# Kernel optimization log

Hardware: AMD Instinct MI355X
Metric: run time of the kernel (lower is better)

## Reference

```python
import jax, jax.numpy as jnp
import numpy as np

N = 100000   # nodes
E = 3200000  # directed edges
F_IN = 128   # data.num_node_features
H = 16       # hidden
C = 2        # output classes (hard-coded in module)


def _glorot(key, fan_in, fan_out):
    s = jnp.sqrt(6.0 / (fan_in + fan_out)).astype(jnp.float32)
    return jax.random.uniform(key, (fan_in, fan_out), jnp.float32, -s, s)


def setup_inputs() -> dict:
    key = jax.random.key(0)
    ks = jax.random.split(key, 5)
    x = jax.random.normal(ks[0], (N, F_IN), jnp.float32)
    edge_index = jax.random.randint(ks[1], (2, E), 0, N, dtype=jnp.int64)
    return {
        "x": x,
        "edge_index": edge_index,
        "W1": _glorot(ks[2], F_IN, H), "b1": jnp.zeros((H,), jnp.float32),
        "W2": _glorot(ks[3], H, H),    "b2": jnp.zeros((H,), jnp.float32),
        "W3": _glorot(ks[4], H, C),    "b3": jnp.zeros((C,), jnp.float32),
    }


def _gcn_conv(x, W, b, src, dst, norm, n):
    # PyG GCNConv: linear transform, then normalized gather -> scatter-add, + bias
    h = x @ W                                   # [N, out]
    msg = h[src] * norm[:, None]                # [E+N, out] gather over source nodes
    out = jax.ops.segment_sum(msg, dst, num_segments=n)  # scatter-add at targets
    return out + b


def reference(x, edge_index, W1, b1, W2, b2, W3, b3):
    n = x.shape[0]
    loop = jnp.arange(n, dtype=edge_index.dtype)
    src = jnp.concatenate([edge_index[0], loop])  # add self-loops (PyG default)
    dst = jnp.concatenate([edge_index[1], loop])
    # symmetric normalization: deg^{-1/2}[src] * deg^{-1/2}[dst], deg = in-degree w/ self-loops
    deg = jax.ops.segment_sum(jnp.ones(src.shape, jnp.float32), dst, num_segments=n)
    dis = jnp.where(deg > 0, jax.lax.rsqrt(jnp.maximum(deg, 1.0)), 0.0)
    norm = dis[src] * dis[dst]
    # dropout is identity in eval mode
    h = jax.nn.relu(_gcn_conv(x, W1, b1, src, dst, norm, n))
    h = jax.nn.relu(_gcn_conv(h, W2, b2, src, dst, norm, n))
    h = _gcn_conv(h, W3, b3, src, dst, norm, n)
    return jax.nn.log_softmax(h, axis=1)
```

## Files before the change

### kernel.cpp

```cpp
#include <hip/hip_runtime.h>
#include <math.h>

#define NSB   512
#define BSH   8
#define BKN   256
#define ESMAX 6272
#define SLOT  10240

typedef _Float16 h8  __attribute__((ext_vector_type(8)));
typedef _Float16 h4  __attribute__((ext_vector_type(4)));
typedef _Float16 h2v __attribute__((ext_vector_type(2)));

__device__ inline int wave_scan_incl(int v) {
    int lane = threadIdx.x & 63;
#pragma unroll
    for (int d = 1; d < 64; d <<= 1) {
        int t = __shfl_up(v, d, 64);
        if (lane >= d) v += t;
    }
    return v;
}


__global__ void k_bucket(const int* __restrict__ src, const int* __restrict__ dst,
                         int* __restrict__ gcur, unsigned* __restrict__ col,
                         int e, int nbuck, int es) {
    __shared__ unsigned sorted[ESMAX];
    __shared__ unsigned char sbuck[ESMAX];
    __shared__ int lc[512], lofE[512], lcur[512], soff[512];
    __shared__ int wsum[8];
    int tid = threadIdx.x;
    lc[tid] = 0;
    __syncthreads();
    int lo = blockIdx.x * es;
    int hi = min(lo + es, e);
    for (int i = lo + tid; i < hi; i += 512)
        atomicAdd(&lc[dst[i] >> BSH], 1);
    __syncthreads();
    int c = lc[tid];
    int inc = wave_scan_incl(c);
    int wid = tid >> 6;
    if ((tid & 63) == 63) wsum[wid] = inc;
    __syncthreads();
    int wofs = 0;
#pragma unroll
    for (int w = 0; w < 8; w++) wofs += (w < wid) ? wsum[w] : 0;
    int excl = inc - c + wofs;
    lofE[tid] = excl;
    lcur[tid] = excl;
    if (tid < nbuck && c > 0)
        soff[tid] = tid * SLOT + atomicAdd(&gcur[tid], c);
    __syncthreads();
    for (int i = lo + tid; i < hi; i += 512) {
        int d = dst[i];
        int b = d >> BSH;
        int p = atomicAdd(&lcur[b], 1);
        sorted[p] = ((unsigned)src[i] << BSH) | (unsigned)(d & (BKN - 1));
        sbuck[p] = (unsigned char)(b & 255);
    }
    __syncthreads();
    int cnt_ = hi - lo;
    int split = (nbuck > 256) ? lofE[256] : 0x7fffffff;
    for (int i = tid; i < cnt_; i += 512) {
        int b = sbuck[i] | ((i >= split) ? 256 : 0);
        col[soff[b] + (i - lofE[b])] = sorted[i];
    }
}


__global__ __launch_bounds__(512) void k_sort(
        const unsigned* __restrict__ col, const int* __restrict__ gcur,
        int* __restrict__ col2, int* __restrict__ rs,
        int* __restrict__ re, float* __restrict__ dis,
        int n, int nbuck) {
    __shared__ int cnt[BKN];
    __shared__ int cur[BKN];
    __shared__ int wsum[4];
    __shared__ int sdat[SLOT];
    int tid = threadIdx.x;
    int b = blockIdx.x;
    int lo = b * SLOT;
    int tot = gcur[b];
    int hi = lo + tot;
    if (tid < BKN) cnt[tid] = 0;
    __syncthreads();
    for (int i = lo + tid; i < hi; i += 512)
        atomicAdd(&cnt[col[i] & (BKN - 1u)], 1);
    __syncthreads();
    int c = (tid < BKN) ? cnt[tid] : 0;
    int inc = wave_scan_incl(c);
    int wid = tid >> 6;
    if (tid < BKN && (tid & 63) == 63) wsum[wid] = inc;
    __syncthreads();
    if (tid < BKN) {
        int wofs = 0;
#pragma unroll
        for (int w = 0; w < 4; w++) wofs += (w < wid) ? wsum[w] : 0;
        int excl = inc - c + wofs;
        cur[tid] = excl;
        int node = (b << BSH) + tid;
        if (node < n) {
            rs[node] = lo + excl;
            re[node] = lo + excl + c;
            dis[node] = rsqrtf((float)(c + 1));
        }
    }
    __syncthreads();
    for (int i = lo + tid; i < hi; i += 512) {
        unsigned v = col[i];
        int pos = atomicAdd(&cur[v & (BKN - 1u)], 1);
        sdat[pos] = (int)(v >> BSH);
    }
    __syncthreads();
    for (int i = tid; i < tot; i += 512)
        col2[lo + i] = sdat[i];
}


__global__ __launch_bounds__(512) void k_linear1s(
        const float* __restrict__ x, const float* __restrict__ W,
        const float* __restrict__ dis, _Float16* __restrict__ hs, int n) {
    __shared__ float sW[2048];
    int tid = threadIdx.x;
    for (int i = tid; i < 2048; i += 512) sW[i] = W[i];
    __syncthreads();
    int cg = tid & 3;
    int kg = (tid >> 2) & 7;
    int nl = tid >> 5;
    float wr[16][4];
#pragma unroll
    for (int j = 0; j < 16; j++)
#pragma unroll
        for (int cc = 0; cc < 4; cc++)
            wr[j][cc] = sW[(kg * 16 + j) * 16 + cg * 4 + cc];
    int nodeBase = blockIdx.x * 128 + nl;
    for (int it = 0; it < 8; it++) {
        int node = nodeBase + it * 16;
        float a0 = 0.f, a1 = 0.f, a2 = 0.f, a3 = 0.f;
        if (node < n) {
            const float4* xr = (const float4*)(x + (size_t)node * 128 + kg * 16);
#pragma unroll
            for (int j4 = 0; j4 < 4; j4++) {
                float4 xv = xr[j4];
                float xs0 = xv.x, xs1 = xv.y, xs2 = xv.z, xs3 = xv.w;
                int j = j4 * 4;
                a0 += xs0 * wr[j][0] + xs1 * wr[j+1][0] + xs2 * wr[j+2][0] + xs3 * wr[j+3][0];
                a1 += xs0 * wr[j][1] + xs1 * wr[j+1][1] + xs2 * wr[j+2][1] + xs3 * wr[j+3][1];
                a2 += xs0 * wr[j][2] + xs1 * wr[j+1][2] + xs2 * wr[j+2][2] + xs3 * wr[j+3][2];
                a3 += xs0 * wr[j][3] + xs1 * wr[j+1][3] + xs2 * wr[j+2][3] + xs3 * wr[j+3][3];
            }
        }
#pragma unroll
        for (int m = 4; m <= 16; m <<= 1) {
            a0 += __shfl_xor(a0, m);
            a1 += __shfl_xor(a1, m);
            a2 += __shfl_xor(a2, m);
            a3 += __shfl_xor(a3, m);
        }
        if (kg == 0 && node < n) {
            float d = dis[node];
            h4 o;
            o[0] = (_Float16)(a0 * d);
            o[1] = (_Float16)(a1 * d);
            o[2] = (_Float16)(a2 * d);
            o[3] = (_Float16)(a3 * d);
            *((h4*)(hs + (size_t)node * 16 + cg * 4)) = o;
        }
    }
}


__global__ __launch_bounds__(256) void k_pullA(
        const _Float16* __restrict__ hs, const int* __restrict__ rs,
        const int* __restrict__ re, const int* __restrict__ col2,
        const float* __restrict__ dis, const float* __restrict__ bb,
        const float* __restrict__ W, _Float16* __restrict__ hsOut, int n) {
    __shared__ float sW[256];
    __shared__ float sb[16];
    if (threadIdx.x < 256) sW[threadIdx.x] = W[threadIdx.x];
    if (threadIdx.x < 16) sb[threadIdx.x] = bb[threadIdx.x];
    __syncthreads();
    long long t = (long long)blockIdx.x * blockDim.x + threadIdx.x;
    int node = (int)(t >> 2), qt = (int)(t & 3);
    if (node >= n) return;
    const h8* H = (const h8*)hs;
    float acc[16];
    if (qt == 0) {
        h8 s0 = H[(size_t)node * 2];
        h8 s1 = H[(size_t)node * 2 + 1];
#pragma unroll
        for (int j = 0; j < 8; j++) { acc[j] = (float)s0[j]; acc[8 + j] = (float)s1[j]; }
    } else {
#pragma unroll
        for (int j = 0; j < 16; j++) acc[j] = 0.f;
    }
    int b = rs[node], e2 = re[node];
    int i = b + qt;
    for (; i + 12 < e2; i += 16) {
        int s0 = col2[i], s1 = col2[i + 4], s2 = col2[i + 8], s3 = col2[i + 12];
        h8 a0 = H[(size_t)s0 * 2], b0 = H[(size_t)s0 * 2 + 1];
        h8 a1 = H[(size_t)s1 * 2], b1 = H[(size_t)s1 * 2 + 1];
        h8 a2 = H[(size_t)s2 * 2], b2 = H[(size_t)s2 * 2 + 1];
        h8 a3 = H[(size_t)s3 * 2], b3 = H[(size_t)s3 * 2 + 1];
#pragma unroll
        for (int j = 0; j < 8; j++) {
            acc[j]     += (float)a0[j] + (float)a1[j] + (float)a2[j] + (float)a3[j];
            acc[8 + j] += (float)b0[j] + (float)b1[j] + (float)b2[j] + (float)b3[j];
        }
    }
    for (; i < e2; i += 4) {
        int s = col2[i];
        h8 a = H[(size_t)s * 2], bq = H[(size_t)s * 2 + 1];
#pragma unroll
        for (int j = 0; j < 8; j++) { acc[j] += (float)a[j]; acc[8 + j] += (float)bq[j]; }
    }
#pragma unroll
    for (int j = 0; j < 16; j++) {
        acc[j] += __shfl_xor(acc[j], 1);
        acc[j] += __shfl_xor(acc[j], 2);
    }
    float d = dis[node];
    float va[16];
#pragma unroll
    for (int k = 0; k < 16; k++) {
        float v = acc[k] * d + sb[k];
        va[k] = v > 0.f ? v : 0.f;
    }
    h4 o;
#pragma unroll
    for (int cc = 0; cc < 4; cc++) {
        int cidx = (qt << 2) + cc;
        float s = 0.f;
#pragma unroll
        for (int k = 0; k < 16; k++) s += va[k] * sW[k * 16 + cidx];
        o[cc] = (_Float16)(s * d);
    }
    *((h4*)(hsOut + (size_t)node * 16 + (qt << 2))) = o;
}


__global__ __launch_bounds__(256) void k_pullB(
        const _Float16* __restrict__ hs, const int* __restrict__ rs,
        const int* __restrict__ re, const int* __restrict__ col2,
        const float* __restrict__ dis, const float* __restrict__ bb,
        const float* __restrict__ W, _Float16* __restrict__ hs2, int n) {
    __shared__ float sW[32];
    __shared__ float sb[16];
    if (threadIdx.x < 32) sW[threadIdx.x] = W[threadIdx.x];
    if (threadIdx.x < 16) sb[threadIdx.x] = bb[threadIdx.x];
    __syncthreads();
    long long t = (long long)blockIdx.x * blockDim.x + threadIdx.x;
    int node = (int)(t >> 2), qt = (int)(t & 3);
    if (node >= n) return;
    const h8* H = (const h8*)hs;
    float acc[16];
    if (qt == 0) {
        h8 s0 = H[(size_t)node * 2];
        h8 s1 = H[(size_t)node * 2 + 1];
#pragma unroll
        for (int j = 0; j < 8; j++) { acc[j] = (float)s0[j]; acc[8 + j] = (float)s1[j]; }
    } else {
#pragma unroll
        for (int j = 0; j < 16; j++) acc[j] = 0.f;
    }
    int b = rs[node], e2 = re[node];
    int i = b + qt;
    for (; i + 12 < e2; i += 16) {
        int s0 = col2[i], s1 = col2[i + 4], s2 = col2[i + 8], s3 = col2[i + 12];
        h8 a0 = H[(size_t)s0 * 2], b0 = H[(size_t)s0 * 2 + 1];
        h8 a1 = H[(size_t)s1 * 2], b1 = H[(size_t)s1 * 2 + 1];
        h8 a2 = H[(size_t)s2 * 2], b2 = H[(size_t)s2 * 2 + 1];
        h8 a3 = H[(size_t)s3 * 2], b3 = H[(size_t)s3 * 2 + 1];
#pragma unroll
        for (int j = 0; j < 8; j++) {
            acc[j]     += (float)a0[j] + (float)a1[j] + (float)a2[j] + (float)a3[j];
            acc[8 + j] += (float)b0[j] + (float)b1[j] + (float)b2[j] + (float)b3[j];
        }
    }
    for (; i < e2; i += 4) {
        int s = col2[i];
        h8 a = H[(size_t)s * 2], bq = H[(size_t)s * 2 + 1];
#pragma unroll
        for (int j = 0; j < 8; j++) { acc[j] += (float)a[j]; acc[8 + j] += (float)bq[j]; }
    }
#pragma unroll
    for (int j = 0; j < 16; j++) {
        acc[j] += __shfl_xor(acc[j], 1);
        acc[j] += __shfl_xor(acc[j], 2);
    }
    float d = dis[node];
    float p0 = 0.f, p1 = 0.f;
#pragma unroll
    for (int k = 0; k < 16; k++) {
        float v = acc[k] * d + sb[k];
        v = v > 0.f ? v : 0.f;
        p0 += v * sW[k * 2 + 0];
        p1 += v * sW[k * 2 + 1];
    }
    if (qt == 0) {
        h2v o;
        o[0] = (_Float16)(p0 * d);
        o[1] = (_Float16)(p1 * d);
        ((h2v*)hs2)[node] = o;
    }
}


__global__ __launch_bounds__(256) void k_pull2lsm(
        const _Float16* __restrict__ hs2, const int* __restrict__ rs,
        const int* __restrict__ re, const int* __restrict__ col2,
        const float* __restrict__ dis, const float* __restrict__ b3,
        float* __restrict__ out, int n) {
    long long t = (long long)blockIdx.x * blockDim.x + threadIdx.x;
    int node = (int)(t >> 2), qt = (int)(t & 3);
    if (node >= n) return;
    const h2v* H = (const h2v*)hs2;
    float a0 = 0.f, a1 = 0.f;
    if (qt == 0) {
        h2v self = H[node];
        a0 = (float)self[0]; a1 = (float)self[1];
    }
    int b = rs[node], e2 = re[node];
    int i = b + qt;
    for (; i + 12 < e2; i += 16) {
        h2v v0 = H[col2[i]];
        h2v v1 = H[col2[i + 4]];
        h2v v2 = H[col2[i + 8]];
        h2v v3 = H[col2[i + 12]];
        a0 += (float)v0[0] + (float)v1[0] + (float)v2[0] + (float)v3[0];
        a1 += (float)v0[1] + (float)v1[1] + (float)v2[1] + (float)v3[1];
    }
    for (; i < e2; i += 4) {
        h2v v = H[col2[i]];
        a0 += (float)v[0];
        a1 += (float)v[1];
    }
    a0 += __shfl_xor(a0, 1); a0 += __shfl_xor(a0, 2);
    a1 += __shfl_xor(a1, 1); a1 += __shfl_xor(a1, 2);
    if (qt == 0) {
        float d = dis[node];
        float z0 = a0 * d + b3[0];
        float z1 = a1 * d + b3[1];
        float m = fmaxf(z0, z1);
        float l = m + logf(expf(z0 - m) + expf(z1 - m));
        float2 o = {z0 - l, z1 - l};
        ((float2*)out)[node] = o;
    }
}


extern "C" void kernel_launch(void* const* d_in, const int* in_sizes, int n_in,
                              void* d_out, int out_size, void* d_ws, size_t ws_size,
                              hipStream_t stream) {
    const float* x  = (const float*)d_in[0];
    const int*   ei = (const int*)d_in[1];
    const float* W1 = (const float*)d_in[2];
    const float* b1 = (const float*)d_in[3];
    const float* W2 = (const float*)d_in[4];
    const float* b2 = (const float*)d_in[5];
    const float* W3 = (const float*)d_in[6];
    const float* b3 = (const float*)d_in[7];
    float* out = (float*)d_out;

    const int N = in_sizes[0] / 128;
    const int E = in_sizes[1] / 2;
    const int* src = ei;
    const int* dst = ei + E;

    const int NBUCK = (N + BKN - 1) >> BSH;
    const int ES = (E + NSB - 1) / NSB;

    char* ws = (char*)d_ws;
    size_t off = 0;
    auto alloc = [&](size_t bytes) {
        void* p = ws + off;
        off += (bytes + 255) & ~(size_t)255;
        return p;
    };
    int*       gcur = (int*)alloc((size_t)NBUCK * sizeof(int));
    unsigned*  col  = (unsigned*)alloc((size_t)NBUCK * SLOT * sizeof(unsigned));
    int*       col2 = (int*)alloc((size_t)NBUCK * SLOT * sizeof(int));
    int*       rs   = (int*)alloc((size_t)N * sizeof(int));
    int*       re   = (int*)alloc((size_t)N * sizeof(int));
    float*     dis  = (float*)alloc((size_t)N * sizeof(float));
    _Float16*  hsA  = (_Float16*)alloc((size_t)N * 16 * sizeof(_Float16));
    _Float16*  hsB  = (_Float16*)alloc((size_t)N * 16 * sizeof(_Float16));
    _Float16*  hs2  = (_Float16*)alloc((size_t)N * 2 * sizeof(_Float16));

    const int B = 256;
    auto g = [&](long long work) { return (int)((work + B - 1) / B); };

    hipMemsetAsync(gcur, 0, (size_t)NBUCK * sizeof(int), stream);
    k_bucket<<<NSB, 512, 0, stream>>>(src, dst, gcur, col, E, NBUCK, ES);
    k_sort<<<NBUCK, 512, 0, stream>>>(col, gcur, col2, rs, re, dis, N, NBUCK);

    k_linear1s<<<(N + 127) / 128, 512, 0, stream>>>(x, W1, dis, hsA, N);

    k_pullA<<<g((long long)N * 4), B, 0, stream>>>(hsA, rs, re, col2, dis, b1, W2, hsB, N);

    k_pullB<<<g((long long)N * 4), B, 0, stream>>>(hsB, rs, re, col2, dis, b2, W3, hs2, N);

    k_pull2lsm<<<g((long long)N * 4), B, 0, stream>>>(hs2, rs, re, col2, dis, b3, out, N);
}
```

Measured before the change: 247.8 us.

## Fuse all pipeline stages into one persistent cooperative kernel with grid syncs

Replaces the memset plus six separate kernel launches with a single cooperative persistent kernel. Grid-stride loops cover each stage, grid-wide barriers separate the stages, and a shared-memory union serves every stage. The aim is to remove per-launch overhead and the idle gaps between the small kernels. In exchange, occupancy is capped by the largest stage's shared-memory footprint and launch bounds, and each grid sync costs time.

```diff
diff --git a/kernel.cpp b/kernel.cpp
--- a/kernel.cpp
+++ b/kernel.cpp
@@ -1,4 +1,5 @@
 #include <hip/hip_runtime.h>
+#include <hip/hip_cooperative_groups.h>
 #include <math.h>
 
 #define NSB   512
@@ -11,6 +12,22 @@
 typedef _Float16 h4  __attribute__((ext_vector_type(4)));
 typedef _Float16 h2v __attribute__((ext_vector_type(2)));
 
+union SU {
+    struct {
+        unsigned sorted[ESMAX];
+        int lc[512], lofE[512], lcur[512], soff[512];
+        int wsum[8];
+        unsigned char sbuck[ESMAX];
+    } b;
+    struct {
+        int sdat[SLOT];
+        int cnt[BKN], cur[BKN];
+        int wsum[4];
+    } s;
+    struct { float sW[2048]; } l;
+    struct { float sW[256]; float sb[16]; } p;
+};
+
 __device__ inline int wave_scan_incl(int v) {
     int lane = threadIdx.x & 63;
 #pragma unroll
@@ -21,330 +38,326 @@
     return v;
 }
 
-
-__global__ void k_bucket(const int* __restrict__ src, const int* __restrict__ dst,
-                         int* __restrict__ gcur, unsigned* __restrict__ col,
-                         int e, int nbuck, int es) {
-    __shared__ unsigned sorted[ESMAX];
-    __shared__ unsigned char sbuck[ESMAX];
-    __shared__ int lc[512], lofE[512], lcur[512], soff[512];
-    __shared__ int wsum[8];
+__device__ inline void gsync(cooperative_groups::grid_group& g) {
+    __threadfence();
+    g.sync();
+    __threadfence();
+}
+
+
+__global__ __launch_bounds__(512, 4) void k_mega(
+        const float* __restrict__ x, const int* __restrict__ srcv, const int* __restrict__ dstv,
+        const float* __restrict__ W1, const float* __restrict__ bias1,
+        const float* __restrict__ W2, const float* __restrict__ bias2,
+        const float* __restrict__ W3, const float* __restrict__ bias3,
+        int* __restrict__ gcur, unsigned* __restrict__ col, int* __restrict__ col2,
+        int* __restrict__ rs, int* __restrict__ re, float* __restrict__ dis,
+        _Float16* __restrict__ hsA, _Float16* __restrict__ hsB, _Float16* __restrict__ hs2,
+        float* __restrict__ out, int n, int e, int nbuck, int es)
+{
+    cooperative_groups::grid_group grid = cooperative_groups::this_grid();
+    __shared__ SU su;
     int tid = threadIdx.x;
-    lc[tid] = 0;
-    __syncthreads();
-    int lo = blockIdx.x * es;
-    int hi = min(lo + es, e);
-    for (int i = lo + tid; i < hi; i += 512)
-        atomicAdd(&lc[dst[i] >> BSH], 1);
-    __syncthreads();
-    int c = lc[tid];
-    int inc = wave_scan_incl(c);
-    int wid = tid >> 6;
-    if ((tid & 63) == 63) wsum[wid] = inc;
-    __syncthreads();
-    int wofs = 0;
-#pragma unroll
-    for (int w = 0; w < 8; w++) wofs += (w < wid) ? wsum[w] : 0;
-    int excl = inc - c + wofs;
-    lofE[tid] = excl;
-    lcur[tid] = excl;
-    if (tid < nbuck && c > 0)
-        soff[tid] = tid * SLOT + atomicAdd(&gcur[tid], c);
-    __syncthreads();
-    for (int i = lo + tid; i < hi; i += 512) {
-        int d = dst[i];
-        int b = d >> BSH;
-        int p = atomicAdd(&lcur[b], 1);
-        sorted[p] = ((unsigned)src[i] << BSH) | (unsigned)(d & (BKN - 1));
-        sbuck[p] = (unsigned char)(b & 255);
-    }
-    __syncthreads();
-    int cnt_ = hi - lo;
-    int split = (nbuck > 256) ? lofE[256] : 0x7fffffff;
-    for (int i = tid; i < cnt_; i += 512) {
-        int b = sbuck[i] | ((i >= split) ? 256 : 0);
-        col[soff[b] + (i - lofE[b])] = sorted[i];
-    }
-}
-
-
-__global__ __launch_bounds__(512) void k_sort(
-        const unsigned* __restrict__ col, const int* __restrict__ gcur,
-        int* __restrict__ col2, int* __restrict__ rs,
-        int* __restrict__ re, float* __restrict__ dis,
-        int n, int nbuck) {
-    __shared__ int cnt[BKN];
-    __shared__ int cur[BKN];
-    __shared__ int wsum[4];
-    __shared__ int sdat[SLOT];
-    int tid = threadIdx.x;
-    int b = blockIdx.x;
-    int lo = b * SLOT;
-    int tot = gcur[b];
-    int hi = lo + tot;
-    if (tid < BKN) cnt[tid] = 0;
-    __syncthreads();
-    for (int i = lo + tid; i < hi; i += 512)
-        atomicAdd(&cnt[col[i] & (BKN - 1u)], 1);
-    __syncthreads();
-    int c = (tid < BKN) ? cnt[tid] : 0;
-    int inc = wave_scan_incl(c);
-    int wid = tid >> 6;
-    if (tid < BKN && (tid & 63) == 63) wsum[wid] = inc;
-    __syncthreads();
-    if (tid < BKN) {
+
+    for (int i = blockIdx.x * 512 + tid; i < nbuck; i += gridDim.x * 512)
+        gcur[i] = 0;
+    gsync(grid);
+
+    for (int blk = blockIdx.x; blk * es < e; blk += gridDim.x) {
+        su.b.lc[tid] = 0;
+        __syncthreads();
+        int lo = blk * es;
+        int hi = min(lo + es, e);
+        for (int i = lo + tid; i < hi; i += 512)
+            atomicAdd(&su.b.lc[dstv[i] >> BSH], 1);
+        __syncthreads();
+        int c = su.b.lc[tid];
+        int inc = wave_scan_incl(c);
+        int wid = tid >> 6;
+        if ((tid & 63) == 63) su.b.wsum[wid] = inc;
+        __syncthreads();
         int wofs = 0;
 #pragma unroll
-        for (int w = 0; w < 4; w++) wofs += (w < wid) ? wsum[w] : 0;
+        for (int w = 0; w < 8; w++) wofs += (w < wid) ? su.b.wsum[w] : 0;
         int excl = inc - c + wofs;
-        cur[tid] = excl;
-        int node = (b << BSH) + tid;
-        if (node < n) {
-            rs[node] = lo + excl;
-            re[node] = lo + excl + c;
-            dis[node] = rsqrtf((float)(c + 1));
-        }
-    }
-    __syncthreads();
-    for (int i = lo + tid; i < hi; i += 512) {
-        unsigned v = col[i];
-        int pos = atomicAdd(&cur[v & (BKN - 1u)], 1);
-        sdat[pos] = (int)(v >> BSH);
-    }
-    __syncthreads();
-    for (int i = tid; i < tot; i += 512)
-        col2[lo + i] = sdat[i];
-}
-
-
-__global__ __launch_bounds__(512) void k_linear1s(
-        const float* __restrict__ x, const float* __restrict__ W,
-        const float* __restrict__ dis, _Float16* __restrict__ hs, int n) {
-    __shared__ float sW[2048];
-    int tid = threadIdx.x;
-    for (int i = tid; i < 2048; i += 512) sW[i] = W[i];
-    __syncthreads();
-    int cg = tid & 3;
-    int kg = (tid >> 2) & 7;
-    int nl = tid >> 5;
-    float wr[16][4];
-#pragma unroll
-    for (int j = 0; j < 16; j++)
-#pragma unroll
-        for (int cc = 0; cc < 4; cc++)
-            wr[j][cc] = sW[(kg * 16 + j) * 16 + cg * 4 + cc];
-    int nodeBase = blockIdx.x * 128 + nl;
-    for (int it = 0; it < 8; it++) {
-        int node = nodeBase + it * 16;
-        float a0 = 0.f, a1 = 0.f, a2 = 0.f, a3 = 0.f;
-        if (node < n) {
-            const float4* xr = (const float4*)(x + (size_t)node * 128 + kg * 16);
-#pragma unroll
-            for (int j4 = 0; j4 < 4; j4++) {
-                float4 xv = xr[j4];
-                float xs0 = xv.x, xs1 = xv.y, xs2 = xv.z, xs3 = xv.w;
-                int j = j4 * 4;
-                a0 += xs0 * wr[j][0] + xs1 * wr[j+1][0] + xs2 * wr[j+2][0] + xs3 * wr[j+3][0];
-                a1 += xs0 * wr[j][1] + xs1 * wr[j+1][1] + xs2 * wr[j+2][1] + xs3 * wr[j+3][1];
-                a2 += xs0 * wr[j][2] + xs1 * wr[j+1][2] + xs2 * wr[j+2][2] + xs3 * wr[j+3][2];
-                a3 += xs0 * wr[j][3] + xs1 * wr[j+1][3] + xs2 * wr[j+2][3] + xs3 * wr[j+3][3];
-            }
-        }
-#pragma unroll
-        for (int m = 4; m <= 16; m <<= 1) {
-            a0 += __shfl_xor(a0, m);
-            a1 += __shfl_xor(a1, m);
-            a2 += __shfl_xor(a2, m);
-            a3 += __shfl_xor(a3, m);
-        }
-        if (kg == 0 && node < n) {
+        su.b.lofE[tid] = excl;
+        su.b.lcur[tid] = excl;
+        if (tid < nbuck && c > 0)
+            su.b.soff[tid] = tid * SLOT + atomicAdd(&gcur[tid], c);
+        __syncthreads();
+        for (int i = lo + tid; i < hi; i += 512) {
+            int d = dstv[i];
+            int bb = d >> BSH;
+            int p = atomicAdd(&su.b.lcur[bb], 1);
+            su.b.sorted[p] = ((unsigned)srcv[i] << BSH) | (unsigned)(d & (BKN - 1));
+            su.b.sbuck[p] = (unsigned char)(bb & 255);
+        }
+        __syncthreads();
+        int cnt_ = hi - lo;
+        int split = (nbuck > 256) ? su.b.lofE[256] : 0x7fffffff;
+        for (int i = tid; i < cnt_; i += 512) {
+            int bb = su.b.sbuck[i] | ((i >= split) ? 256 : 0);
+            col[su.b.soff[bb] + (i - su.b.lofE[bb])] = su.b.sorted[i];
+        }
+        __syncthreads();
+    }
+    gsync(grid);
+
+    for (int bk = blockIdx.x; bk < nbuck; bk += gridDim.x) {
+        int lo = bk * SLOT;
+        int tot = gcur[bk];
+        int hi = lo + tot;
+        if (tid < BKN) su.s.cnt[tid] = 0;
+        __syncthreads();
+        for (int i = lo + tid; i < hi; i += 512)
+            atomicAdd(&su.s.cnt[col[i] & (BKN - 1u)], 1);
+        __syncthreads();
+        int c = (tid < BKN) ? su.s.cnt[tid] : 0;
+        int inc = wave_scan_incl(c);
+        int wid = tid >> 6;
+        if (tid < BKN && (tid & 63) == 63) su.s.wsum[wid] = inc;
+        __syncthreads();
+        if (tid < BKN) {
+            int wofs = 0;
+#pragma unroll
+            for (int w = 0; w < 4; w++) wofs += (w < wid) ? su.s.wsum[w] : 0;
+            int excl = inc - c + wofs;
+            su.s.cur[tid] = excl;
+            int node = (bk << BSH) + tid;
+            if (node < n) {
+                rs[node] = lo + excl;
+                re[node] = lo + excl + c;
+                dis[node] = rsqrtf((float)(c + 1));
+            }
+        }
+        __syncthreads();
+        for (int i = lo + tid; i < hi; i += 512) {
+            unsigned v = col[i];
+            int pos = atomicAdd(&su.s.cur[v & (BKN - 1u)], 1);
+            su.s.sdat[pos] = (int)(v >> BSH);
+        }
+        __syncthreads();
+        for (int i = tid; i < tot; i += 512)
+            col2[lo + i] = su.s.sdat[i];
+        __syncthreads();
+    }
+    gsync(grid);
+
+    {
+        for (int i = tid; i < 2048; i += 512) su.l.sW[i] = W1[i];
+        __syncthreads();
+        int cgi = tid & 3;
+        int kg = (tid >> 2) & 7;
+        int nl = tid >> 5;
+        float wr[16][4];
+#pragma unroll
+        for (int j = 0; j < 16; j++)
+#pragma unroll
+            for (int cc = 0; cc < 4; cc++)
+                wr[j][cc] = su.l.sW[(kg * 16 + j) * 16 + cgi * 4 + cc];
+        for (int base = blockIdx.x * 128; base < n; base += gridDim.x * 128) {
+            int nodeBase = base + nl;
+            for (int it = 0; it < 8; it++) {
+                int node = nodeBase + it * 16;
+                float a0 = 0.f, a1 = 0.f, a2 = 0.f, a3 = 0.f;
+                if (node < n) {
+                    const float4* xr = (const float4*)(x + (size_t)node * 128 + kg * 16);
+#pragma unroll
+                    for (int j4 = 0; j4 < 4; j4++) {
+                        float4 xv = xr[j4];
+                        float xs0 = xv.x, xs1 = xv.y, xs2 = xv.z, xs3 = xv.w;
+                        int j = j4 * 4;
+                        a0 += xs0 * wr[j][0] + xs1 * wr[j+1][0] + xs2 * wr[j+2][0] + xs3 * wr[j+3][0];
+                        a1 += xs0 * wr[j][1] + xs1 * wr[j+1][1] + xs2 * wr[j+2][1] + xs3 * wr[j+3][1];
+                        a2 += xs0 * wr[j][2] + xs1 * wr[j+1][2] + xs2 * wr[j+2][2] + xs3 * wr[j+3][2];
+                        a3 += xs0 * wr[j][3] + xs1 * wr[j+1][3] + xs2 * wr[j+2][3] + xs3 * wr[j+3][3];
+                    }
+                }
+#pragma unroll
+                for (int m = 4; m <= 16; m <<= 1) {
+                    a0 += __shfl_xor(a0, m);
+                    a1 += __shfl_xor(a1, m);
+                    a2 += __shfl_xor(a2, m);
+                    a3 += __shfl_xor(a3, m);
+                }
+                if (kg == 0 && node < n) {
+                    float d = dis[node];
+                    h4 o;
+                    o[0] = (_Float16)(a0 * d);
+                    o[1] = (_Float16)(a1 * d);
+                    o[2] = (_Float16)(a2 * d);
+                    o[3] = (_Float16)(a3 * d);
+                    *((h4*)(hsA + (size_t)node * 16 + cgi * 4)) = o;
+                }
+            }
+        }
+    }
+    gsync(grid);
+
+    {
+        if (tid < 256) su.p.sW[tid] = W2[tid];
+        if (tid < 16)  su.p.sb[tid] = bias1[tid];
+        __syncthreads();
+        const h8* H = (const h8*)hsA;
+        long long stride = (long long)gridDim.x * 512;
+        for (long long t = (long long)blockIdx.x * 512 + tid; (t >> 2) < (long long)n; t += stride) {
+            int node = (int)(t >> 2), qt = (int)(t & 3);
+            float acc[16];
+            if (qt == 0) {
+                h8 s0 = H[(size_t)node * 2];
+                h8 s1 = H[(size_t)node * 2 + 1];
+#pragma unroll
+                for (int j = 0; j < 8; j++) { acc[j] = (float)s0[j]; acc[8 + j] = (float)s1[j]; }
+            } else {
+#pragma unroll
+                for (int j = 0; j < 16; j++) acc[j] = 0.f;
+            }
+            int b0i = rs[node], e2 = re[node];
+            int i = b0i + qt;
+            for (; i + 12 < e2; i += 16) {
+                int s0 = col2[i], s1 = col2[i + 4], s2 = col2[i + 8], s3 = col2[i + 12];
+                h8 y0 = H[(size_t)s0 * 2], z0 = H[(size_t)s0 * 2 + 1];
+                h8 y1 = H[(size_t)s1 * 2], z1 = H[(size_t)s1 * 2 + 1];
+                h8 y2 = H[(size_t)s2 * 2], z2 = H[(size_t)s2 * 2 + 1];
+                h8 y3 = H[(size_t)s3 * 2], z3 = H[(size_t)s3 * 2 + 1];
+#pragma unroll
+                for (int j = 0; j < 8; j++) {
+                    acc[j]     += (float)y0[j] + (float)y1[j] + (float)y2[j] + (float)y3[j];
+                    acc[8 + j] += (float)z0[j] + (float)z1[j] + (float)z2[j] + (float)z3[j];
+                }
+            }
+            for (; i < e2; i += 4) {
+                int s = col2[i];
+                h8 y = H[(size_t)s * 2], z = H[(size_t)s * 2 + 1];
+#pragma unroll
+                for (int j = 0; j < 8; j++) { acc[j] += (float)y[j]; acc[8 + j] += (float)z[j]; }
+            }
+#pragma unroll
+            for (int j = 0; j < 16; j++) {
+                acc[j] += __shfl_xor(acc[j], 1);
+                acc[j] += __shfl_xor(acc[j], 2);
+            }
             float d = dis[node];
+            float va[16];
+#pragma unroll
+            for (int k = 0; k < 16; k++) {
+                float v = acc[k] * d + su.p.sb[k];
+                va[k] = v > 0.f ? v : 0.f;
+            }
             h4 o;
-            o[0] = (_Float16)(a0 * d);
-            o[1] = (_Float16)(a1 * d);
-            o[2] = (_Float16)(a2 * d);
-            o[3] = (_Float16)(a3 * d);
-            *((h4*)(hs + (size_t)node * 16 + cg * 4)) = o;
-        }
-    }
-}
-
-
-__global__ __launch_bounds__(256) void k_pullA(
-        const _Float16* __restrict__ hs, const int* __restrict__ rs,
-        const int* __restrict__ re, const int* __restrict__ col2,
-        const float* __restrict__ dis, const float* __restrict__ bb,
-        const float* __restrict__ W, _Float16* __restrict__ hsOut, int n) {
-    __shared__ float sW[256];
-    __shared__ float sb[16];
-    if (threadIdx.x < 256) sW[threadIdx.x] = W[threadIdx.x];
-    if (threadIdx.x < 16) sb[threadIdx.x] = bb[threadIdx.x];
-    __syncthreads();
-    long long t = (long long)blockIdx.x * blockDim.x + threadIdx.x;
-    int node = (int)(t >> 2), qt = (int)(t & 3);
-    if (node >= n) return;
-    const h8* H = (const h8*)hs;
-    float acc[16];
-    if (qt == 0) {
-        h8 s0 = H[(size_t)node * 2];
-        h8 s1 = H[(size_t)node * 2 + 1];
-#pragma unroll
-        for (int j = 0; j < 8; j++) { acc[j] = (float)s0[j]; acc[8 + j] = (float)s1[j]; }
-    } else {
-#pragma unroll
-        for (int j = 0; j < 16; j++) acc[j] = 0.f;
-    }
-    int b = rs[node], e2 = re[node];
-    int i = b + qt;
-    for (; i + 12 < e2; i += 16) {
-        int s0 = col2[i], s1 = col2[i + 4], s2 = col2[i + 8], s3 = col2[i + 12];
-        h8 a0 = H[(size_t)s0 * 2], b0 = H[(size_t)s0 * 2 + 1];
-        h8 a1 = H[(size_t)s1 * 2], b1 = H[(size_t)s1 * 2 + 1];
-        h8 a2 = H[(size_t)s2 * 2], b2 = H[(size_t)s2 * 2 + 1];
-        h8 a3 = H[(size_t)s3 * 2], b3 = H[(size_t)s3 * 2 + 1];
-#pragma unroll
-        for (int j = 0; j < 8; j++) {
-            acc[j]     += (float)a0[j] + (float)a1[j] + (float)a2[j] + (float)a3[j];
-            acc[8 + j] += (float)b0[j] + (float)b1[j] + (float)b2[j] + (float)b3[j];
-        }
-    }
-    for (; i < e2; i += 4) {
-        int s = col2[i];
-        h8 a = H[(size_t)s * 2], bq = H[(size_t)s * 2 + 1];
-#pragma unroll
-        for (int j = 0; j < 8; j++) { acc[j] += (float)a[j]; acc[8 + j] += (float)bq[j]; }
-    }
-#pragma unroll
-    for (int j = 0; j < 16; j++) {
-        acc[j] += __shfl_xor(acc[j], 1);
-        acc[j] += __shfl_xor(acc[j], 2);
-    }
-    float d = dis[node];
-    float va[16];
-#pragma unroll
-    for (int k = 0; k < 16; k++) {
-        float v = acc[k] * d + sb[k];
-        va[k] = v > 0.f ? v : 0.f;
-    }
-    h4 o;
-#pragma unroll
-    for (int cc = 0; cc < 4; cc++) {
-        int cidx = (qt << 2) + cc;
-        float s = 0.f;
-#pragma unroll
-        for (int k = 0; k < 16; k++) s += va[k] * sW[k * 16 + cidx];
-        o[cc] = (_Float16)(s * d);
-    }
-    *((h4*)(hsOut + (size_t)node * 16 + (qt << 2))) = o;
-}
-
-
-__global__ __launch_bounds__(256) void k_pullB(
-        const _Float16* __restrict__ hs, const int* __restrict__ rs,
-        const int* __restrict__ re, const int* __restrict__ col2,
-        const float* __restrict__ dis, const float* __restrict__ bb,
-        const float* __restrict__ W, _Float16* __restrict__ hs2, int n) {
-    __shared__ float sW[32];
-    __shared__ float sb[16];
-    if (threadIdx.x < 32) sW[threadIdx.x] = W[threadIdx.x];
-    if (threadIdx.x < 16) sb[threadIdx.x] = bb[threadIdx.x];
-    __syncthreads();
-    long long t = (long long)blockIdx.x * blockDim.x + threadIdx.x;
-    int node = (int)(t >> 2), qt = (int)(t & 3);
-    if (node >= n) return;
-    const h8* H = (const h8*)hs;
-    float acc[16];
-    if (qt == 0) {
-        h8 s0 = H[(size_t)node * 2];
-        h8 s1 = H[(size_t)node * 2 + 1];
-#pragma unroll
-        for (int j = 0; j < 8; j++) { acc[j] = (float)s0[j]; acc[8 + j] = (float)s1[j]; }
-    } else {
-#pragma unroll
-        for (int j = 0; j < 16; j++) acc[j] = 0.f;
-    }
-    int b = rs[node], e2 = re[node];
-    int i = b + qt;
-    for (; i + 12 < e2; i += 16) {
-        int s0 = col2[i], s1 = col2[i + 4], s2 = col2[i + 8], s3 = col2[i + 12];
-        h8 a0 = H[(size_t)s0 * 2], b0 = H[(size_t)s0 * 2 + 1];
-        h8 a1 = H[(size_t)s1 * 2], b1 = H[(size_t)s1 * 2 + 1];
-        h8 a2 = H[(size_t)s2 * 2], b2 = H[(size_t)s2 * 2 + 1];
-        h8 a3 = H[(size_t)s3 * 2], b3 = H[(size_t)s3 * 2 + 1];
-#pragma unroll
-        for (int j = 0; j < 8; j++) {
-            acc[j]     += (float)a0[j] + (float)a1[j] + (float)a2[j] + (float)a3[j];
-            acc[8 + j] += (float)b0[j] + (float)b1[j] + (float)b2[j] + (float)b3[j];
-        }
-    }
-    for (; i < e2; i += 4) {
-        int s = col2[i];
-        h8 a = H[(size_t)s * 2], bq = H[(size_t)s * 2 + 1];
-#pragma unroll
-        for (int j = 0; j < 8; j++) { acc[j] += (float)a[j]; acc[8 + j] += (float)bq[j]; }
-    }
-#pragma unroll
-    for (int j = 0; j < 16; j++) {
-        acc[j] += __shfl_xor(acc[j], 1);
-        acc[j] += __shfl_xor(acc[j], 2);
-    }
-    float d = dis[node];
-    float p0 = 0.f, p1 = 0.f;
-#pragma unroll
-    for (int k = 0; k < 16; k++) {
-        float v = acc[k] * d + sb[k];
-        v = v > 0.f ? v : 0.f;
-        p0 += v * sW[k * 2 + 0];
-        p1 += v * sW[k * 2 + 1];
-    }
-    if (qt == 0) {
-        h2v o;
-        o[0] = (_Float16)(p0 * d);
-        o[1] = (_Float16)(p1 * d);
-        ((h2v*)hs2)[node] = o;
-    }
-}
-
-
-__global__ __launch_bounds__(256) void k_pull2lsm(
-        const _Float16* __restrict__ hs2, const int* __restrict__ rs,
-        const int* __restrict__ re, const int* __restrict__ col2,
-        const float* __restrict__ dis, const float* __restrict__ b3,
-        float* __restrict__ out, int n) {
-    long long t = (long long)blockIdx.x * blockDim.x + threadIdx.x;
-    int node = (int)(t >> 2), qt = (int)(t & 3);
-    if (node >= n) return;
-    const h2v* H = (const h2v*)hs2;
-    float a0 = 0.f, a1 = 0.f;
-    if (qt == 0) {
-        h2v self = H[node];
-        a0 = (float)self[0]; a1 = (float)self[1];
-    }
-    int b = rs[node], e2 = re[node];
-    int i = b + qt;
-    for (; i + 12 < e2; i += 16) {
-        h2v v0 = H[col2[i]];
-        h2v v1 = H[col2[i + 4]];
-        h2v v2 = H[col2[i + 8]];
-        h2v v3 = H[col2[i + 12]];
-        a0 += (float)v0[0] + (float)v1[0] + (float)v2[0] + (float)v3[0];
-        a1 += (float)v0[1] + (float)v1[1] + (float)v2[1] + (float)v3[1];
-    }
-    for (; i < e2; i += 4) {
-        h2v v = H[col2[i]];
-        a0 += (float)v[0];
-        a1 += (float)v[1];
-    }
-    a0 += __shfl_xor(a0, 1); a0 += __shfl_xor(a0, 2);
-    a1 += __shfl_xor(a1, 1); a1 += __shfl_xor(a1, 2);
-    if (qt == 0) {
-        float d = dis[node];
-        float z0 = a0 * d + b3[0];
-        float z1 = a1 * d + b3[1];
-        float m = fmaxf(z0, z1);
-        float l = m + logf(expf(z0 - m) + expf(z1 - m));
-        float2 o = {z0 - l, z1 - l};
-        ((float2*)out)[node] = o;
+#pragma unroll
+            for (int cc = 0; cc < 4; cc++) {
+                int cidx = (qt << 2) + cc;
+                float s = 0.f;
+#pragma unroll
+                for (int k = 0; k < 16; k++) s += va[k] * su.p.sW[k * 16 + cidx];
+                o[cc] = (_Float16)(s * d);
+            }
+            *((h4*)(hsB + (size_t)node * 16 + (qt << 2))) = o;
+        }
+    }
+    gsync(grid);
+
+    {
+        if (tid < 32) su.p.sW[tid] = W3[tid];
+        if (tid < 16) su.p.sb[tid] = bias2[tid];
+        __syncthreads();
+        const h8* H = (const h8*)hsB;
+        long long stride = (long long)gridDim.x * 512;
+        for (long long t = (long long)blockIdx.x * 512 + tid; (t >> 2) < (long long)n; t += stride) {
+            int node = (int)(t >> 2), qt = (int)(t & 3);
+            float acc[16];
+            if (qt == 0) {
+                h8 s0 = H[(size_t)node * 2];
+                h8 s1 = H[(size_t)node * 2 + 1];
+#pragma unroll
+                for (int j = 0; j < 8; j++) { acc[j] = (float)s0[j]; acc[8 + j] = (float)s1[j]; }
+            } else {
+#pragma unroll
+                for (int j = 0; j < 16; j++) acc[j] = 0.f;
+            }
+            int b0i = rs[node], e2 = re[node];
+            int i = b0i + qt;
+            for (; i + 12 < e2; i += 16) {
+                int s0 = col2[i], s1 = col2[i + 4], s2 = col2[i + 8], s3 = col2[i + 12];
+                h8 y0 = H[(size_t)s0 * 2], z0 = H[(size_t)s0 * 2 + 1];
+                h8 y1 = H[(size_t)s1 * 2], z1 = H[(size_t)s1 * 2 + 1];
+                h8 y2 = H[(size_t)s2 * 2], z2 = H[(size_t)s2 * 2 + 1];
+                h8 y3 = H[(size_t)s3 * 2], z3 = H[(size_t)s3 * 2 + 1];
+#pragma unroll
+                for (int j = 0; j < 8; j++) {
+                    acc[j]     += (float)y0[j] + (float)y1[j] + (float)y2[j] + (float)y3[j];
+                    acc[8 + j] += (float)z0[j] + (float)z1[j] + (float)z2[j] + (float)z3[j];
+                }
+            }
+            for (; i < e2; i += 4) {
+                int s = col2[i];
+                h8 y = H[(size_t)s * 2], z = H[(size_t)s * 2 + 1];
+#pragma unroll
+                for (int j = 0; j < 8; j++) { acc[j] += (float)y[j]; acc[8 + j] += (float)z[j]; }
+            }
+#pragma unroll
+            for (int j = 0; j < 16; j++) {
+                acc[j] += __shfl_xor(acc[j], 1);
+                acc[j] += __shfl_xor(acc[j], 2);
+            }
+            float d = dis[node];
+            float p0 = 0.f, p1 = 0.f;
+#pragma unroll
+            for (int k = 0; k < 16; k++) {
+                float v = acc[k] * d + su.p.sb[k];
+                v = v > 0.f ? v : 0.f;
+                p0 += v * su.p.sW[k * 2 + 0];
+                p1 += v * su.p.sW[k * 2 + 1];
+            }
+            if (qt == 0) {
+                h2v o;
+                o[0] = (_Float16)(p0 * d);
+                o[1] = (_Float16)(p1 * d);
+                ((h2v*)hs2)[node] = o;
+            }
+        }
+    }
+    gsync(grid);
+
+    {
+        const h2v* H = (const h2v*)hs2;
+        float bz0 = bias3[0], bz1 = bias3[1];
+        long long stride = (long long)gridDim.x * 512;
+        for (long long t = (long long)blockIdx.x * 512 + tid; (t >> 2) < (long long)n; t += stride) {
+            int node = (int)(t >> 2), qt = (int)(t & 3);
+            float a0 = 0.f, a1 = 0.f;
+            if (qt == 0) {
+                h2v self = H[node];
+                a0 = (float)self[0]; a1 = (float)self[1];
+            }
+            int b0i = rs[node], e2 = re[node];
+            int i = b0i + qt;
+            for (; i + 12 < e2; i += 16) {
+                h2v v0 = H[col2[i]];
+                h2v v1 = H[col2[i + 4]];
+                h2v v2 = H[col2[i + 8]];
+                h2v v3 = H[col2[i + 12]];
+                a0 += (float)v0[0] + (float)v1[0] + (float)v2[0] + (float)v3[0];
+                a1 += (float)v0[1] + (float)v1[1] + (float)v2[1] + (float)v3[1];
+            }
+            for (; i < e2; i += 4) {
+                h2v v = H[col2[i]];
+                a0 += (float)v[0];
+                a1 += (float)v[1];
+            }
+            a0 += __shfl_xor(a0, 1); a0 += __shfl_xor(a0, 2);
+            a1 += __shfl_xor(a1, 1); a1 += __shfl_xor(a1, 2);
+            if (qt == 0) {
+                float d = dis[node];
+                float z0 = a0 * d + bz0;
+                float z1 = a1 * d + bz1;
+                float m = fmaxf(z0, z1);
+                float l = m + logf(expf(z0 - m) + expf(z1 - m));
+                float2 o = {z0 - l, z1 - l};
+                ((float2*)out)[node] = o;
+            }
+        }
     }
 }
 
@@ -362,13 +375,13 @@
     const float* b3 = (const float*)d_in[7];
     float* out = (float*)d_out;
 
-    const int N = in_sizes[0] / 128;
-    const int E = in_sizes[1] / 2;
+    int N = in_sizes[0] / 128;
+    int E = in_sizes[1] / 2;
     const int* src = ei;
     const int* dst = ei + E;
 
-    const int NBUCK = (N + BKN - 1) >> BSH;
-    const int ES = (E + NSB - 1) / NSB;
+    int NBUCK = (N + BKN - 1) >> BSH;
+    int ES = (E + NSB - 1) / NSB;
 
     char* ws = (char*)d_ws;
     size_t off = 0;
@@ -387,18 +400,23 @@
     _Float16*  hsB  = (_Float16*)alloc((size_t)N * 16 * sizeof(_Float16));
     _Float16*  hs2  = (_Float16*)alloc((size_t)N * 2 * sizeof(_Float16));
 
-    const int B = 256;
-    auto g = [&](long long work) { return (int)((work + B - 1) / B); };
-
-    hipMemsetAsync(gcur, 0, (size_t)NBUCK * sizeof(int), stream);
-    k_bucket<<<NSB, 512, 0, stream>>>(src, dst, gcur, col, E, NBUCK, ES);
-    k_sort<<<NBUCK, 512, 0, stream>>>(col, gcur, col2, rs, re, dis, N, NBUCK);
-
-    k_linear1s<<<(N + 127) / 128, 512, 0, stream>>>(x, W1, dis, hsA, N);
-
-    k_pullA<<<g((long long)N * 4), B, 0, stream>>>(hsA, rs, re, col2, dis, b1, W2, hsB, N);
-
-    k_pullB<<<g((long long)N * 4), B, 0, stream>>>(hsB, rs, re, col2, dis, b2, W3, hs2, N);
-
-    k_pull2lsm<<<g((long long)N * 4), B, 0, stream>>>(hs2, rs, re, col2, dis, b3, out, N);
+    static int gridBlocks = 0;
+    if (gridBlocks == 0) {
+        int mb = 0;
+        if (hipOccupancyMaxActiveBlocksPerMultiprocessor(&mb, k_mega, 512, 0) != hipSuccess || mb < 1)
+            mb = 2;
+        int ncu = 256;
+        int dev = 0;
+        hipGetDevice(&dev);
+        hipDeviceGetAttribute(&ncu, hipDeviceAttributeMultiprocessorCount, dev);
+        long long g = (long long)mb * ncu;
+        if (g > 1024) g = 1024;
+        gridBlocks = (int)g;
+    }
+
+    void* args[] = { &x, &src, &dst, &W1, &b1, &W2, &b2, &W3, &b3,
+                     &gcur, &col, &col2, &rs, &re, &dis, &hsA, &hsB, &hs2,
+                     &out, &N, &E, &NBUCK, &ES };
+    hipLaunchCooperativeKernel((void*)k_mega, dim3(gridBlocks), dim3(512),
+                               args, 0, stream);
 }
```

Result: slower. 898.3 us (+262.5%).

## Overlap first-layer linear with edge bucketing in one fused launch

Applied to the files above, without the earlier changes.

The edge-bucketing kernel and the first linear transform are merged into one launch with a block-index split. The extra blocks compute an unnormalized x@W1 while the bucket blocks run, so the two independent stages share the device instead of running back to back. Scaling by deg^-1/2 moves into the sort kernel, which also writes col2 straight to global memory instead of staging it in shared memory. The cost is an extra fp16 round trip through an hsRaw buffer and a larger shared-memory union that may reduce occupancy for the linear blocks.

```diff
diff --git a/kernel.cpp b/kernel.cpp
--- a/kernel.cpp
+++ b/kernel.cpp
@@ -22,66 +22,122 @@
 }
 
 
-__global__ void k_bucket(const int* __restrict__ src, const int* __restrict__ dst,
-                         int* __restrict__ gcur, unsigned* __restrict__ col,
-                         int e, int nbuck, int es) {
-    __shared__ unsigned sorted[ESMAX];
-    __shared__ unsigned char sbuck[ESMAX];
-    __shared__ int lc[512], lofE[512], lcur[512], soff[512];
-    __shared__ int wsum[8];
+union BU {
+    struct {
+        unsigned sorted[ESMAX];
+        int lc[512], lofE[512], lcur[512], soff[512];
+        int wsum[8];
+        unsigned char sbuck[ESMAX];
+    } b;
+    struct { float sW[2048]; } l;
+};
+
+__global__ __launch_bounds__(512) void k_build(
+        const int* __restrict__ srcv, const int* __restrict__ dstv,
+        const float* __restrict__ x, const float* __restrict__ W1,
+        int* __restrict__ gcur, unsigned* __restrict__ col,
+        _Float16* __restrict__ hsRaw,
+        int e, int nbuck, int es, int n, int nlin) {
+    __shared__ BU su;
     int tid = threadIdx.x;
-    lc[tid] = 0;
-    __syncthreads();
-    int lo = blockIdx.x * es;
-    int hi = min(lo + es, e);
-    for (int i = lo + tid; i < hi; i += 512)
-        atomicAdd(&lc[dst[i] >> BSH], 1);
-    __syncthreads();
-    int c = lc[tid];
-    int inc = wave_scan_incl(c);
-    int wid = tid >> 6;
-    if ((tid & 63) == 63) wsum[wid] = inc;
-    __syncthreads();
-    int wofs = 0;
-#pragma unroll
-    for (int w = 0; w < 8; w++) wofs += (w < wid) ? wsum[w] : 0;
-    int excl = inc - c + wofs;
-    lofE[tid] = excl;
-    lcur[tid] = excl;
-    if (tid < nbuck && c > 0)
-        soff[tid] = tid * SLOT + atomicAdd(&gcur[tid], c);
-    __syncthreads();
-    for (int i = lo + tid; i < hi; i += 512) {
-        int d = dst[i];
-        int b = d >> BSH;
-        int p = atomicAdd(&lcur[b], 1);
-        sorted[p] = ((unsigned)src[i] << BSH) | (unsigned)(d & (BKN - 1));
-        sbuck[p] = (unsigned char)(b & 255);
-    }
-    __syncthreads();
-    int cnt_ = hi - lo;
-    int split = (nbuck > 256) ? lofE[256] : 0x7fffffff;
-    for (int i = tid; i < cnt_; i += 512) {
-        int b = sbuck[i] | ((i >= split) ? 256 : 0);
-        col[soff[b] + (i - lofE[b])] = sorted[i];
-    }
-}
-
-
-__global__ __launch_bounds__(512) void k_sort(
+
+    if (blockIdx.x < NSB) {
+        su.b.lc[tid] = 0;
+        __syncthreads();
+        int lo = blockIdx.x * es;
+        int hi = min(lo + es, e);
+        for (int i = lo + tid; i < hi; i += 512)
+            atomicAdd(&su.b.lc[dstv[i] >> BSH], 1);
+        __syncthreads();
+        int c = su.b.lc[tid];
+        int inc = wave_scan_incl(c);
+        int wid = tid >> 6;
+        if ((tid & 63) == 63) su.b.wsum[wid] = inc;
+        __syncthreads();
+        int wofs = 0;
+#pragma unroll
+        for (int w = 0; w < 8; w++) wofs += (w < wid) ? su.b.wsum[w] : 0;
+        int excl = inc - c + wofs;
+        su.b.lofE[tid] = excl;
+        su.b.lcur[tid] = excl;
+        if (tid < nbuck && c > 0)
+            su.b.soff[tid] = tid * SLOT + atomicAdd(&gcur[tid], c);
+        __syncthreads();
+        for (int i = lo + tid; i < hi; i += 512) {
+            int d = dstv[i];
+            int bb = d >> BSH;
+            int p = atomicAdd(&su.b.lcur[bb], 1);
+            su.b.sorted[p] = ((unsigned)srcv[i] << BSH) | (unsigned)(d & (BKN - 1));
+            su.b.sbuck[p] = (unsigned char)(bb & 255);
+        }
+        __syncthreads();
+        int cnt_ = hi - lo;
+        int split = (nbuck > 256) ? su.b.lofE[256] : 0x7fffffff;
+        for (int i = tid; i < cnt_; i += 512) {
+            int bb = su.b.sbuck[i] | ((i >= split) ? 256 : 0);
+            col[su.b.soff[bb] + (i - su.b.lofE[bb])] = su.b.sorted[i];
+        }
+    } else {
+        for (int i = tid; i < 2048; i += 512) su.l.sW[i] = W1[i];
+        __syncthreads();
+        int cgi = tid & 3;
+        int kg  = (tid >> 2) & 15;
+        int wv  = tid >> 6;
+        float wr[8][4];
+#pragma unroll
+        for (int j = 0; j < 8; j++)
+#pragma unroll
+            for (int cc = 0; cc < 4; cc++)
+                wr[j][cc] = su.l.sW[(kg * 8 + j) * 16 + cgi * 4 + cc];
+        int lb = blockIdx.x - NSB;
+        for (int base = lb * 8; base < n; base += nlin * 8) {
+            int node = base + wv;
+            float a0 = 0.f, a1 = 0.f, a2 = 0.f, a3 = 0.f;
+            if (node < n) {
+                const float4* xr = (const float4*)(x + (size_t)node * 128 + kg * 8);
+                float4 xv0 = xr[0], xv1 = xr[1];
+                float xs[8] = {xv0.x, xv0.y, xv0.z, xv0.w, xv1.x, xv1.y, xv1.z, xv1.w};
+#pragma unroll
+                for (int j = 0; j < 8; j++) {
+                    a0 += xs[j] * wr[j][0];
+                    a1 += xs[j] * wr[j][1];
+                    a2 += xs[j] * wr[j][2];
+                    a3 += xs[j] * wr[j][3];
+                }
+            }
+#pragma unroll
+            for (int m = 4; m <= 32; m <<= 1) {
+                a0 += __shfl_xor(a0, m);
+                a1 += __shfl_xor(a1, m);
+                a2 += __shfl_xor(a2, m);
+                a3 += __shfl_xor(a3, m);
+            }
+            if (kg == 0 && node < n) {
+                h4 o;
+                o[0] = (_Float16)a0;
+                o[1] = (_Float16)a1;
+                o[2] = (_Float16)a2;
+                o[3] = (_Float16)a3;
+                *((h4*)(hsRaw + (size_t)node * 16 + cgi * 4)) = o;
+            }
+        }
+    }
+}
+
+
+__global__ __launch_bounds__(512) void k_sort2(
         const unsigned* __restrict__ col, const int* __restrict__ gcur,
         int* __restrict__ col2, int* __restrict__ rs,
         int* __restrict__ re, float* __restrict__ dis,
-        int n, int nbuck) {
+        const _Float16* __restrict__ hsRaw, _Float16* __restrict__ hsA, int n) {
     __shared__ int cnt[BKN];
     __shared__ int cur[BKN];
     __shared__ int wsum[4];
-    __shared__ int sdat[SLOT];
+    __shared__ float sdis[BKN];
     int tid = threadIdx.x;
-    int b = blockIdx.x;
-    int lo = b * SLOT;
-    int tot = gcur[b];
-    int hi = lo + tot;
+    int bk = blockIdx.x;
+    int lo = bk * SLOT;
+    int hi = lo + gcur[bk];
     if (tid < BKN) cnt[tid] = 0;
     __syncthreads();
     for (int i = lo + tid; i < hi; i += 512)
@@ -97,74 +153,31 @@
 #pragma unroll
         for (int w = 0; w < 4; w++) wofs += (w < wid) ? wsum[w] : 0;
         int excl = inc - c + wofs;
-        cur[tid] = excl;
-        int node = (b << BSH) + tid;
+        cur[tid] = lo + excl;
+        float d = rsqrtf((float)(c + 1));
+        sdis[tid] = d;
+        int node = (bk << BSH) + tid;
         if (node < n) {
             rs[node] = lo + excl;
             re[node] = lo + excl + c;
-            dis[node] = rsqrtf((float)(c + 1));
+            dis[node] = d;
         }
     }
     __syncthreads();
     for (int i = lo + tid; i < hi; i += 512) {
         unsigned v = col[i];
         int pos = atomicAdd(&cur[v & (BKN - 1u)], 1);
-        sdat[pos] = (int)(v >> BSH);
-    }
-    __syncthreads();
-    for (int i = tid; i < tot; i += 512)
-        col2[lo + i] = sdat[i];
-}
-
-
-__global__ __launch_bounds__(512) void k_linear1s(
-        const float* __restrict__ x, const float* __restrict__ W,
-        const float* __restrict__ dis, _Float16* __restrict__ hs, int n) {
-    __shared__ float sW[2048];
-    int tid = threadIdx.x;
-    for (int i = tid; i < 2048; i += 512) sW[i] = W[i];
-    __syncthreads();
-    int cg = tid & 3;
-    int kg = (tid >> 2) & 7;
-    int nl = tid >> 5;
-    float wr[16][4];
-#pragma unroll
-    for (int j = 0; j < 16; j++)
-#pragma unroll
-        for (int cc = 0; cc < 4; cc++)
-            wr[j][cc] = sW[(kg * 16 + j) * 16 + cg * 4 + cc];
-    int nodeBase = blockIdx.x * 128 + nl;
-    for (int it = 0; it < 8; it++) {
-        int node = nodeBase + it * 16;
-        float a0 = 0.f, a1 = 0.f, a2 = 0.f, a3 = 0.f;
+        col2[pos] = (int)(v >> BSH);
+    }
+    {
+        int node = (bk << BSH) + (tid >> 1);
         if (node < n) {
-            const float4* xr = (const float4*)(x + (size_t)node * 128 + kg * 16);
-#pragma unroll
-            for (int j4 = 0; j4 < 4; j4++) {
-                float4 xv = xr[j4];
-                float xs0 = xv.x, xs1 = xv.y, xs2 = xv.z, xs3 = xv.w;
-                int j = j4 * 4;
-                a0 += xs0 * wr[j][0] + xs1 * wr[j+1][0] + xs2 * wr[j+2][0] + xs3 * wr[j+3][0];
-                a1 += xs0 * wr[j][1] + xs1 * wr[j+1][1] + xs2 * wr[j+2][1] + xs3 * wr[j+3][1];
-                a2 += xs0 * wr[j][2] + xs1 * wr[j+1][2] + xs2 * wr[j+2][2] + xs3 * wr[j+3][2];
-                a3 += xs0 * wr[j][3] + xs1 * wr[j+1][3] + xs2 * wr[j+2][3] + xs3 * wr[j+3][3];
-            }
-        }
-#pragma unroll
-        for (int m = 4; m <= 16; m <<= 1) {
-            a0 += __shfl_xor(a0, m);
-            a1 += __shfl_xor(a1, m);
-            a2 += __shfl_xor(a2, m);
-            a3 += __shfl_xor(a3, m);
-        }
-        if (kg == 0 && node < n) {
-            float d = dis[node];
-            h4 o;
-            o[0] = (_Float16)(a0 * d);
-            o[1] = (_Float16)(a1 * d);
-            o[2] = (_Float16)(a2 * d);
-            o[3] = (_Float16)(a3 * d);
-            *((h4*)(hs + (size_t)node * 16 + cg * 4)) = o;
+            float d = sdis[tid >> 1];
+            h8 v = ((const h8*)hsRaw)[(size_t)node * 2 + (tid & 1)];
+            h8 o;
+#pragma unroll
+            for (int j = 0; j < 8; j++) o[j] = (_Float16)((float)v[j] * d);
+            ((h8*)hsA)[(size_t)node * 2 + (tid & 1)] = o;
         }
     }
 }
@@ -369,6 +382,7 @@
 
     const int NBUCK = (N + BKN - 1) >> BSH;
     const int ES = (E + NSB - 1) / NSB;
+    const int NLIN = (N + 127) / 128;
 
     char* ws = (char*)d_ws;
     size_t off = 0;
@@ -377,24 +391,26 @@
         off += (bytes + 255) & ~(size_t)255;
         return p;
     };
-    int*       gcur = (int*)alloc((size_t)NBUCK * sizeof(int));
-    unsigned*  col  = (unsigned*)alloc((size_t)NBUCK * SLOT * sizeof(unsigned));
-    int*       col2 = (int*)alloc((size_t)NBUCK * SLOT * sizeof(int));
-    int*       rs   = (int*)alloc((size_t)N * sizeof(int));
-    int*       re   = (int*)alloc((size_t)N * sizeof(int));
-    float*     dis  = (float*)alloc((size_t)N * sizeof(float));
-    _Float16*  hsA  = (_Float16*)alloc((size_t)N * 16 * sizeof(_Float16));
-    _Float16*  hsB  = (_Float16*)alloc((size_t)N * 16 * sizeof(_Float16));
-    _Float16*  hs2  = (_Float16*)alloc((size_t)N * 2 * sizeof(_Float16));
+    int*       gcur  = (int*)alloc((size_t)NBUCK * sizeof(int));
+    unsigned*  col   = (unsigned*)alloc((size_t)NBUCK * SLOT * sizeof(unsigned));
+    int*       col2  = (int*)alloc((size_t)NBUCK * SLOT * sizeof(int));
+    int*       rs    = (int*)alloc((size_t)N * sizeof(int));
+    int*       re    = (int*)alloc((size_t)N * sizeof(int));
+    float*     dis   = (float*)alloc((size_t)N * sizeof(float));
+    _Float16*  hsRaw = (_Float16*)alloc((size_t)N * 16 * sizeof(_Float16));
+    _Float16*  hsA   = (_Float16*)alloc((size_t)N * 16 * sizeof(_Float16));
+    _Float16*  hsB   = (_Float16*)alloc((size_t)N * 16 * sizeof(_Float16));
+    _Float16*  hs2   = (_Float16*)alloc((size_t)N * 2 * sizeof(_Float16));
 
     const int B = 256;
     auto g = [&](long long work) { return (int)((work + B - 1) / B); };
 
     hipMemsetAsync(gcur, 0, (size_t)NBUCK * sizeof(int), stream);
-    k_bucket<<<NSB, 512, 0, stream>>>(src, dst, gcur, col, E, NBUCK, ES);
-    k_sort<<<NBUCK, 512, 0, stream>>>(col, gcur, col2, rs, re, dis, N, NBUCK);
-
-    k_linear1s<<<(N + 127) / 128, 512, 0, stream>>>(x, W1, dis, hsA, N);
+
+    k_build<<<NSB + NLIN, 512, 0, stream>>>(src, dst, x, W1, gcur, col, hsRaw,
+                                            E, NBUCK, ES, N, NLIN);
+
+    k_sort2<<<NBUCK, 512, 0, stream>>>(col, gcur, col2, rs, re, dis, hsRaw, hsA, N);
 
     k_pullA<<<g((long long)N * 4), B, 0, stream>>>(hsA, rs, re, col2, dis, b1, W2, hsB, N);
 
```

New measurement: 261.1 us. +5.4%, slower.
